# Optimization experiments

Measured on AMD Instinct MI355X. Metric: run time of the kernel, lower is better.

Reference implementation:

```python
import jax, jax.numpy as jnp
import numpy as np

D_MODEL = 1024
N_HEADS = 16
D_K = D_MODEL // N_HEADS
B, S = 4, 2048


def setup_inputs() -> dict:
    key = jax.random.key(0)
    ks = jax.random.split(key, 9)
    sc = 1.0 / np.sqrt(D_MODEL)
    inp = {
        "x": jax.random.normal(ks[0], (B, S, D_MODEL), dtype=jnp.float32),
        # causal mask, broadcastable over batch and heads; 0 -> masked
        "mask": jnp.tril(jnp.ones((S, S), dtype=jnp.int32))[None, None, :, :],
        "Wq": jax.random.normal(ks[1], (D_MODEL, D_MODEL), dtype=jnp.float32) * sc,
        "bq": jax.random.normal(ks[2], (D_MODEL,), dtype=jnp.float32) * sc,
        "Wk": jax.random.normal(ks[3], (D_MODEL, D_MODEL), dtype=jnp.float32) * sc,
        "bk": jax.random.normal(ks[4], (D_MODEL,), dtype=jnp.float32) * sc,
        "Wv": jax.random.normal(ks[5], (D_MODEL, D_MODEL), dtype=jnp.float32) * sc,
        "bv": jax.random.normal(ks[6], (D_MODEL,), dtype=jnp.float32) * sc,
        "Wo": jax.random.normal(ks[7], (D_MODEL, D_MODEL), dtype=jnp.float32) * sc,
        "bo": jax.random.normal(ks[8], (D_MODEL,), dtype=jnp.float32) * sc,
    }
    return inp


def _split_heads(t):
    b, s, _ = t.shape
    return t.reshape(b, s, N_HEADS, D_K).transpose(0, 2, 1, 3)  # [B,H,S,dk]


def reference(x, mask, Wq, bq, Wk, bk, Wv, bv, Wo, bo):
    Q = _split_heads(x @ Wq.T + bq)
    K = _split_heads(x @ Wk.T + bk)
    V = _split_heads(x @ Wv.T + bv)
    scores = jnp.einsum("bhqd,bhkd->bhqk", Q, K) / jnp.sqrt(jnp.float32(D_K))
    scores = jnp.where(mask == 0, jnp.float32(-1e9), scores)
    weights = jax.nn.softmax(scores, axis=-1)
    attn = jnp.einsum("bhqk,bhkd->bhqd", weights, V)  # [B,H,S,dk]
    attn = attn.transpose(0, 2, 1, 3).reshape(x.shape[0], x.shape[1], D_MODEL)
    return attn @ Wo.T + bo
```

## Files before the change

### kernel.cpp

```cpp
#include <hip/hip_runtime.h>
#include <hip/hip_bf16.h>
#include <cstdint>

#define DM   1024
#define NH   16
#define DK   64
#define BB   4
#define SS   2048
#define MTOT (BB * SS)
#define PAD  68

typedef short short8 __attribute__((ext_vector_type(8)));
typedef float f32x4  __attribute__((ext_vector_type(4)));
using u16 = unsigned short;

__device__ inline u16 f2b(float f) {
    union { float f; unsigned int u; } v; v.f = f;
    unsigned int u = v.u;
    u += 0x7fffu + ((u >> 16) & 1u);
    return (u16)(u >> 16);
}
__device__ inline float b2f(u16 s) {
    union { unsigned int u; float f; } v; v.u = ((unsigned int)s) << 16;
    return v.f;
}
__device__ inline unsigned int pack2(float lo, float hi) {
    union { float f; unsigned int u; } a, b; a.f = lo; b.f = hi;
    return (b.u & 0xFFFF0000u) | (a.u >> 16);
}

__device__ inline void load_lds16(const u16* g, u16* l) {
    __builtin_amdgcn_global_load_lds(
        (const __attribute__((address_space(1))) unsigned int*)g,
        (__attribute__((address_space(3))) unsigned int*)l, 16, 0, 0);
}

struct CvtPtrs {
    const void *x, *Wq, *Wk, *Wv, *Wo, *bq, *bk, *bv, *bo;
    u16 *xb, *Wqb, *Wkb, *Wvb, *Wob, *bqb, *bkb, *bvb, *bob;
};

__global__ void convert_all(CvtPtrs p, int* __restrict__ flag)
{
    __shared__ int cnt;
    if (threadIdx.x == 0) cnt = 0;
    __syncthreads();
    int c = 0;
    for (int i = threadIdx.x; i < 512; i += 256) {
        const int e = (((const u16*)p.x)[i] >> 7) & 0xFF;
        if (e >= 100 && e <= 140) c++;
    }
    atomicAdd(&cnt, c);
    __syncthreads();
    const int isbf = (cnt >= 420) ? 1 : 0;
    if (blockIdx.x == 0 && threadIdx.x == 0) *flag = isbf;
    if (isbf) return;

    const size_t E  = (size_t)MTOT * DM;
    const size_t W1 = (size_t)DM * DM;
    const size_t i = ((size_t)blockIdx.x * blockDim.x + threadIdx.x) * 8;
    const float* s; u16* d; size_t off;
    if (i < E) {
        s = (const float*)p.x; d = p.xb; off = i;
    } else {
        size_t j = i - E;
        if (j < (W1 << 2)) {
            const int w = (int)(j >> 20); off = j & (W1 - 1);
            const float* ss[4] = {(const float*)p.Wq, (const float*)p.Wk,
                                  (const float*)p.Wv, (const float*)p.Wo};
            u16* dd[4] = {p.Wqb, p.Wkb, p.Wvb, p.Wob};
            s = ss[w]; d = dd[w];
        } else {
            j -= (W1 << 2);
            if (j >= 4 * DM) return;
            const int w = (int)(j >> 10); off = j & (DM - 1);
            const float* ss[4] = {(const float*)p.bq, (const float*)p.bk,
                                  (const float*)p.bv, (const float*)p.bo};
            u16* dd[4] = {p.bqb, p.bkb, p.bvb, p.bob};
            s = ss[w]; d = dd[w];
        }
    }
    const float4 f0 = *(const float4*)(s + off);
    const float4 f1 = *(const float4*)(s + off + 4);
    u16 tmp[8] = {f2b(f0.x), f2b(f0.y), f2b(f0.z), f2b(f0.w),
                  f2b(f1.x), f2b(f1.y), f2b(f1.z), f2b(f1.w)};
    *(int4*)(d + off) = *(const int4*)tmp;
}

__device__ __forceinline__
void gemm_body(const u16* __restrict__ A, const u16* __restrict__ Bw,
               const u16* __restrict__ bias, void* __restrict__ out,
               int mode, float scale, int isbf, int m0, int n0,
               u16 (*As)[64], u16 (*Bs)[64])
{
    const int tid  = threadIdx.x;
    const int wave = tid >> 6;
    const int lane = tid & 63;
    const int wm = (wave >> 1) * 64;
    const int wn = (wave & 1) * 64;

    const int lm   = lane & 15;
    const int quad = lane >> 4;
    const int kq   = quad * 8;
    const int rq   = quad * 4;

    const int lrow   = lane >> 3;
    const int lchunk = (lane & 7) ^ lrow;
    const u16* gA = A  + (size_t)(m0 + 8*wave + lrow) * DM + lchunk * 8;
    const u16* gB = Bw + (size_t)(n0 + 8*wave + lrow) * DM + lchunk * 8;
    u16* ldsA = (u16*)((char*)&As[0][0] + wave * 1024);
    u16* ldsB = (u16*)((char*)&Bs[0][0] + wave * 1024);

    f32x4 acc[4][4] = {};

    for (int k0 = 0; k0 < DM; k0 += 64) {
        __syncthreads();
#pragma unroll
        for (int c = 0; c < 4; c++) {
            load_lds16(gA + (size_t)c*32*DM + k0, (u16*)((char*)ldsA + c*4096));
            load_lds16(gB + (size_t)c*32*DM + k0, (u16*)((char*)ldsB + c*4096));
        }
        __syncthreads();

#pragma unroll
        for (int ks = 0; ks < 2; ks++) {
            const int ca = ((ks*4 + quad) ^ (lm & 7)) * 8;
            short8 af[4], bf[4];
#pragma unroll
            for (int i = 0; i < 4; i++) af[i] = *(const short8*)(&As[wm + 16*i + lm][ca]);
#pragma unroll
            for (int j = 0; j < 4; j++) bf[j] = *(const short8*)(&Bs[wn + 16*j + lm][ca]);
#pragma unroll
            for (int i = 0; i < 4; i++)
#pragma unroll
                for (int j = 0; j < 4; j++)
                    acc[i][j] = __builtin_amdgcn_mfma_f32_16x16x32_bf16(af[i], bf[j], acc[i][j], 0, 0, 0);
        }
    }

#pragma unroll
    for (int j = 0; j < 4; j++) {
        const int col = n0 + wn + 16*j + lm;
        const float bv = b2f(bias[col]);
        const int h = col >> 6, d = col & 63;
#pragma unroll
        for (int i = 0; i < 4; i++) {
            if (mode == 2) {
                const int row0 = m0 + wm + 16*i + rq;
                const int b = row0 >> 11, s = row0 & 2047;
                u16 tmp[4];
#pragma unroll
                for (int r = 0; r < 4; r++)
                    tmp[r] = f2b((acc[i][j][r] + bv) * scale);
                const size_t idx = (((size_t)(b*NH + h) * DK) + d) * SS + s;
                *(uint2*)(&((u16*)out)[idx]) = *(const uint2*)tmp;
            } else {
#pragma unroll
                for (int r = 0; r < 4; r++) {
                    const int row = m0 + wm + 16*i + rq + r;
                    const float v = (acc[i][j][r] + bv) * scale;
                    if (mode == 0) {
                        const size_t idx = (size_t)row * DM + col;
                        if (isbf) ((u16*)out)[idx] = f2b(v);
                        else      ((float*)out)[idx] = v;
                    } else {
                        const int b = row >> 11, s = row & 2047;
                        const size_t idx = (((size_t)(b*NH + h) * SS) + s) * DK + d;
                        ((u16*)out)[idx] = f2b(v);
                    }
                }
            }
        }
    }
}

__global__ __launch_bounds__(256)
void gemm_qkv(CvtPtrs p, u16* __restrict__ Qb, u16* __restrict__ Kb,
              u16* __restrict__ Vb, float qscale, const int* __restrict__ flag)
{
    __shared__ __align__(16) u16 As[128][64];
    __shared__ __align__(16) u16 Bs[128][64];
    const int id  = blockIdx.x;
    const int xcd = id & 7;
    const int j   = id >> 3;
    const int m0  = (xcd * 8 + (j & 7)) * 128;
    const int n0  = ((j >> 3) & 7) * 128;
    const int z   = j >> 6;
    const int isbf = *flag;
    const u16* A = isbf ? (const u16*)p.x : p.xb;
    const u16* Bw, *bias; u16* out;
    if (z == 0)      { Bw = isbf ? (const u16*)p.Wq : p.Wqb; bias = isbf ? (const u16*)p.bq : p.bqb; out = Qb; }
    else if (z == 1) { Bw = isbf ? (const u16*)p.Wk : p.Wkb; bias = isbf ? (const u16*)p.bk : p.bkb; out = Kb; }
    else             { Bw = isbf ? (const u16*)p.Wv : p.Wvb; bias = isbf ? (const u16*)p.bv : p.bvb; out = Vb; }
    const int mode  = (z == 2) ? 2 : 1;
    const float sc  = (z == 0) ? qscale : 1.0f;
    gemm_body(A, Bw, bias, out, mode, sc, 1, m0, n0, As, Bs);
}

__global__ __launch_bounds__(256)
void gemm_out(const u16* __restrict__ Ab, CvtPtrs p, void* __restrict__ out,
              const int* __restrict__ flag)
{
    __shared__ __align__(16) u16 As[128][64];
    __shared__ __align__(16) u16 Bs[128][64];
    const int id  = blockIdx.x;
    const int xcd = id & 7;
    const int j   = id >> 3;
    const int m0  = (xcd * 8 + (j & 7)) * 128;
    const int n0  = (j >> 3) * 128;
    const int isbf = *flag;
    const u16* Bw   = isbf ? (const u16*)p.Wo : p.Wob;
    const u16* bias = isbf ? (const u16*)p.bo : p.bob;
    gemm_body(Ab, Bw, bias, out, 0, 1.0f, isbf, m0, n0, As, Bs);
}

__global__ __launch_bounds__(256)
void attn_causal(const u16* __restrict__ Q, const u16* __restrict__ K,
                 const u16* __restrict__ VT, u16* __restrict__ O)
{
    __shared__ __align__(16) u16 Ks[2][64][PAD];
    __shared__ __align__(16) u16 Vs[2][64][PAD];
    __shared__ __align__(16) u16 Ps[128][PAD];

    const int tid  = threadIdx.x;
    const int wave = tid >> 6;
    const int lane = tid & 63;
    const int qx = blockIdx.x;
    const int h = blockIdx.y, b = blockIdx.z;
    const int bh = b * NH + h;

    const u16* Kg = K  + (size_t)bh * SS * DK;
    const u16* Vg = VT + (size_t)bh * DK * SS;

    const int srow = tid >> 3;
    const int scol = (tid & 7) * 8;
    const int lm = lane & 15, quad = lane >> 4, kq = quad * 8, rq = quad * 4;

#pragma unroll
    for (int seg = 0; seg < 2; seg++) {
        const int qt = seg ? (15 - qx) : qx;
        const int q0 = qt * 128;
        const int nt = 2 * (qt + 1);
        const u16* Qg = Q + ((size_t)bh * SS + q0) * DK;

        short8 qa[2][2];
#pragma unroll
        for (int mi = 0; mi < 2; mi++)
#pragma unroll
            for (int ks = 0; ks < 2; ks++)
                qa[mi][ks] = *(const short8*)(&Qg[(size_t)(32*wave + 16*mi + lm) * DK + ks*32 + kq]);

        int4 kv0 = *(const int4*)(&Kg[(size_t)srow * DK + scol]);
        int4 kv1 = *(const int4*)(&Kg[(size_t)(srow + 32) * DK + scol]);
        int4 vv0 = *(const int4*)(&Vg[(size_t)srow * SS + scol]);
        int4 vv1 = *(const int4*)(&Vg[(size_t)(srow + 32) * SS + scol]);
        *(int4*)(&Ks[0][srow][scol])      = kv0;
        *(int4*)(&Ks[0][srow + 32][scol]) = kv1;
        *(int4*)(&Vs[0][srow][scol])      = vv0;
        *(int4*)(&Vs[0][srow + 32][scol]) = vv1;
        __syncthreads();

        kv0 = *(const int4*)(&Kg[(size_t)(64 + srow) * DK + scol]);
        kv1 = *(const int4*)(&Kg[(size_t)(64 + srow + 32) * DK + scol]);
        vv0 = *(const int4*)(&Vg[(size_t)srow * SS + 64 + scol]);
        vv1 = *(const int4*)(&Vg[(size_t)(srow + 32) * SS + 64 + scol]);

        f32x4 o[2][4] = {};
        float lacc[2] = {0.f, 0.f};

        for (int t = 0; t < nt; t++) {
            const int buf = t & 1;
            const int k0 = 64 * t;

            f32x4 sw[2][4] = {};
            __builtin_amdgcn_s_setprio(1);
#pragma unroll
            for (int ks = 0; ks < 2; ks++)
#pragma unroll
                for (int j = 0; j < 4; j++) {
                    const short8 kfr = *(const short8*)(&Ks[buf][16*j + lm][ks*32 + kq]);
                    sw[0][j] = __builtin_amdgcn_mfma_f32_16x16x32_bf16(kfr, qa[0][ks], sw[0][j], 0, 0, 0);
                    sw[1][j] = __builtin_amdgcn_mfma_f32_16x16x32_bf16(kfr, qa[1][ks], sw[1][j], 0, 0, 0);
                }
            __builtin_amdgcn_s_setprio(0);

            if (k0 + 63 > q0 + 32*wave) {
#pragma unroll
                for (int mi = 0; mi < 2; mi++)
#pragma unroll
                    for (int j = 0; j < 4; j++)
#pragma unroll
                        for (int r = 0; r < 4; r++)
                            if (k0 + 16*j + rq + r > q0 + 32*wave + 16*mi + lm)
                                sw[mi][j][r] = -1e30f;
            }

#pragma unroll
            for (int mi = 0; mi < 2; mi++) {
#pragma unroll
                for (int j = 0; j < 4; j++) {
                    const float p0 = __builtin_amdgcn_exp2f(sw[mi][j][0]);
                    const float p1 = __builtin_amdgcn_exp2f(sw[mi][j][1]);
                    const float p2 = __builtin_amdgcn_exp2f(sw[mi][j][2]);
                    const float p3 = __builtin_amdgcn_exp2f(sw[mi][j][3]);
                    lacc[mi] += (p0 + p1) + (p2 + p3);
                    uint2 w; w.x = pack2(p0, p1); w.y = pack2(p2, p3);
                    *(uint2*)(&Ps[32*wave + 16*mi + lm][16*j + rq]) = w;
                }
            }

            __builtin_amdgcn_s_setprio(1);
#pragma unroll
            for (int ks = 0; ks < 2; ks++) {
                const short8 pa0 = *(const short8*)(&Ps[32*wave + lm][ks*32 + kq]);
                const short8 pa1 = *(const short8*)(&Ps[32*wave + 16 + lm][ks*32 + kq]);
#pragma unroll
                for (int j = 0; j < 4; j++) {
                    const short8 vfr = *(const short8*)(&Vs[buf][16*j + lm][ks*32 + kq]);
                    o[0][j] = __builtin_amdgcn_mfma_f32_16x16x32_bf16(pa0, vfr, o[0][j], 0, 0, 0);
                    o[1][j] = __builtin_amdgcn_mfma_f32_16x16x32_bf16(pa1, vfr, o[1][j], 0, 0, 0);
                }
            }
            __builtin_amdgcn_s_setprio(0);

            if (t + 1 < nt) {
                const int nb = buf ^ 1;
                *(int4*)(&Ks[nb][srow][scol])      = kv0;
                *(int4*)(&Ks[nb][srow + 32][scol]) = kv1;
                *(int4*)(&Vs[nb][srow][scol])      = vv0;
                *(int4*)(&Vs[nb][srow + 32][scol]) = vv1;
                if (t + 2 < nt) {
                    const int kn = 64 * (t + 2);
                    kv0 = *(const int4*)(&Kg[(size_t)(kn + srow) * DK + scol]);
                    kv1 = *(const int4*)(&Kg[(size_t)(kn + srow + 32) * DK + scol]);
                    vv0 = *(const int4*)(&Vg[(size_t)srow * SS + kn + scol]);
                    vv1 = *(const int4*)(&Vg[(size_t)(srow + 32) * SS + kn + scol]);
                }
            }
            __syncthreads();
        }

#pragma unroll
        for (int mi = 0; mi < 2; mi++) {
            lacc[mi] += __shfl_xor(lacc[mi], 16, 64);
            lacc[mi] += __shfl_xor(lacc[mi], 32, 64);
        }

#pragma unroll
        for (int mi = 0; mi < 2; mi++)
#pragma unroll
            for (int r = 0; r < 4; r++) {
                const float rs = __shfl(lacc[mi], (lane & 48) + rq + r, 64);
                const float inv = 1.f / rs;
                const size_t rowg = (size_t)b * SS + q0 + 32*wave + 16*mi + rq + r;
#pragma unroll
                for (int j = 0; j < 4; j++)
                    O[rowg * DM + h*DK + 16*j + lm] = f2b(o[mi][j][r] * inv);
            }
    }
}

extern "C" void kernel_launch(void* const* d_in, const int* in_sizes, int n_in,
                              void* d_out, int out_size, void* d_ws, size_t ws_size,
                              hipStream_t stream)
{
    (void)in_sizes; (void)n_in; (void)out_size; (void)ws_size;

    int* flag = (int*)d_ws;
    u16* ws = (u16*)((char*)d_ws + 16);

    const size_t E  = (size_t)MTOT * DM;
    const size_t W1 = (size_t)DM * DM;
    u16* xb  = ws;
    u16* Wqb = ws + E;
    u16* Wkb = Wqb + W1;
    u16* Wvb = Wkb + W1;
    u16* Wob = Wvb + W1;
    u16* bqb = Wob + W1;
    u16* bkb = bqb + DM;
    u16* bvb = bkb + DM;
    u16* bob = bvb + DM;
    u16* Qb  = bob + DM;
    u16* Kb  = Qb + E;
    u16* Vb  = Kb + E;
    u16* Ab  = xb;

    CvtPtrs p;
    p.x = d_in[0];
    p.Wq = d_in[2]; p.bq = d_in[3];
    p.Wk = d_in[4]; p.bk = d_in[5];
    p.Wv = d_in[6]; p.bv = d_in[7];
    p.Wo = d_in[8]; p.bo = d_in[9];
    p.xb = xb;
    p.Wqb = Wqb; p.Wkb = Wkb; p.Wvb = Wvb; p.Wob = Wob;
    p.bqb = bqb; p.bkb = bkb; p.bvb = bvb; p.bob = bob;

    const int cvt_blocks = (int)((E + 4*W1 + 4*DM) / 2048);
    convert_all<<<cvt_blocks, 256, 0, stream>>>(p, flag);

    const float qscale = 0.18033688011112042f;

    gemm_qkv<<<1536, 256, 0, stream>>>(p, Qb, Kb, Vb, qscale, flag);
    attn_causal<<<dim3(SS/256, NH, BB), 256, 0, stream>>>(Qb, Kb, Vb, Ab);
    gemm_out<<<512, 256, 0, stream>>>(Ab, p, d_out, flag);
}
```

Before: 285.7 us.

## Load K/V fragments directly from global into registers, drop LDS staging and barriers

The attention kernel no longer stages K and V tiles through shared memory with block-wide barriers. Each wave loads its own MFMA fragments straight from global memory, double-buffering K fragments in registers one tile ahead. Each wave also runs its own causal tile count, so it skips tiles that lie fully above its diagonal. This removes the LDS round trip and the __syncthreads stalls, but each wave now loads K/V redundantly (four times the global/L2 traffic), V loads are not prefetched, and register pressure rises.

```diff
diff --git a/kernel.cpp b/kernel.cpp
--- a/kernel.cpp
+++ b/kernel.cpp
@@ -214,12 +214,79 @@
     gemm_body(Ab, Bw, bias, out, 0, 1.0f, isbf, m0, n0, As, Bs);
 }
 
+
+#define PREF_K(dst, kt) do {                                                    \
+    const int _pk0 = (kt) * 64;                                                 \
+    _Pragma("unroll")                                                           \
+    for (int _pj = 0; _pj < 4; _pj++) {                                         \
+        dst[_pj]     = *(const short8*)(&Kg[(size_t)(_pk0 + 16*_pj + lm)*DK + kq]);      \
+        dst[4 + _pj] = *(const short8*)(&Kg[(size_t)(_pk0 + 16*_pj + lm)*DK + 32 + kq]); \
+    }                                                                           \
+} while (0)
+
+#define TILE_BODY(kt, KF) do {                                                  \
+    const int _k0 = (kt) * 64;                                                  \
+                   \
+    short8 _vf[8];                                                              \
+    _Pragma("unroll")                                                           \
+    for (int _j = 0; _j < 4; _j++) {                                            \
+        _vf[_j]     = *(const short8*)(&Vg[(size_t)(16*_j + lm)*SS + _k0 + kq]);      \
+        _vf[4 + _j] = *(const short8*)(&Vg[(size_t)(16*_j + lm)*SS + _k0 + 32 + kq]); \
+    }                                                                           \
+       \
+    f32x4 _sw[2][4] = {};                                                       \
+    __builtin_amdgcn_s_setprio(1);                                              \
+    _Pragma("unroll")                                                           \
+    for (int _ks = 0; _ks < 2; _ks++)                                           \
+        _Pragma("unroll")                                                       \
+        for (int _j = 0; _j < 4; _j++) {                                        \
+            _sw[0][_j] = __builtin_amdgcn_mfma_f32_16x16x32_bf16(KF[_ks*4+_j], qa[0][_ks], _sw[0][_j], 0, 0, 0); \
+            _sw[1][_j] = __builtin_amdgcn_mfma_f32_16x16x32_bf16(KF[_ks*4+_j], qa[1][_ks], _sw[1][_j], 0, 0, 0); \
+        }                                                                       \
+    __builtin_amdgcn_s_setprio(0);                                              \
+    if (_k0 + 63 > q0 + 32*wave) {                                              \
+        _Pragma("unroll")                                                       \
+        for (int _mi = 0; _mi < 2; _mi++)                                       \
+            _Pragma("unroll")                                                   \
+            for (int _j = 0; _j < 4; _j++)                                      \
+                _Pragma("unroll")                                               \
+                for (int _r = 0; _r < 4; _r++)                                  \
+                    if (_k0 + 16*_j + rq + _r > q0 + 32*wave + 16*_mi + lm)     \
+                        _sw[_mi][_j][_r] = -1e30f;                              \
+    }                                                                           \
+          \
+    _Pragma("unroll")                                                           \
+    for (int _mi = 0; _mi < 2; _mi++) {                                         \
+        _Pragma("unroll")                                                       \
+        for (int _j = 0; _j < 4; _j++) {                                        \
+            const float _p0 = __builtin_amdgcn_exp2f(_sw[_mi][_j][0]);          \
+            const float _p1 = __builtin_amdgcn_exp2f(_sw[_mi][_j][1]);          \
+            const float _p2 = __builtin_amdgcn_exp2f(_sw[_mi][_j][2]);          \
+            const float _p3 = __builtin_amdgcn_exp2f(_sw[_mi][_j][3]);          \
+            lacc[_mi] += (_p0 + _p1) + (_p2 + _p3);                             \
+            uint2 _w; _w.x = pack2(_p0, _p1); _w.y = pack2(_p2, _p3);           \
+            *(uint2*)(&Ps[32*wave + 16*_mi + lm][16*_j + rq]) = _w;             \
+        }                                                                       \
+    }                                                                           \
+                 \
+    __builtin_amdgcn_s_setprio(1);                                              \
+    _Pragma("unroll")                                                           \
+    for (int _ks = 0; _ks < 2; _ks++) {                                         \
+        const short8 _pa0 = *(const short8*)(&Ps[32*wave + lm][_ks*32 + kq]);   \
+        const short8 _pa1 = *(const short8*)(&Ps[32*wave + 16 + lm][_ks*32 + kq]); \
+        _Pragma("unroll")                                                       \
+        for (int _j = 0; _j < 4; _j++) {                                        \
+            o[0][_j] = __builtin_amdgcn_mfma_f32_16x16x32_bf16(_pa0, _vf[_ks*4+_j], o[0][_j], 0, 0, 0); \
+            o[1][_j] = __builtin_amdgcn_mfma_f32_16x16x32_bf16(_pa1, _vf[_ks*4+_j], o[1][_j], 0, 0, 0); \
+        }                                                                       \
+    }                                                                           \
+    __builtin_amdgcn_s_setprio(0);                                              \
+} while (0)
+
 __global__ __launch_bounds__(256)
 void attn_causal(const u16* __restrict__ Q, const u16* __restrict__ K,
                  const u16* __restrict__ VT, u16* __restrict__ O)
 {
-    __shared__ __align__(16) u16 Ks[2][64][PAD];
-    __shared__ __align__(16) u16 Vs[2][64][PAD];
     __shared__ __align__(16) u16 Ps[128][PAD];
 
     const int tid  = threadIdx.x;
@@ -232,15 +299,13 @@
     const u16* Kg = K  + (size_t)bh * SS * DK;
     const u16* Vg = VT + (size_t)bh * DK * SS;
 
-    const int srow = tid >> 3;
-    const int scol = (tid & 7) * 8;
     const int lm = lane & 15, quad = lane >> 4, kq = quad * 8, rq = quad * 4;
 
 #pragma unroll
     for (int seg = 0; seg < 2; seg++) {
         const int qt = seg ? (15 - qx) : qx;
         const int q0 = qt * 128;
-        const int nt = 2 * (qt + 1);
+        const int ntw = (q0 + 32*wave + 95) >> 6;
         const u16* Qg = Q + ((size_t)bh * SS + q0) * DK;
 
         short8 qa[2][2];
@@ -250,94 +315,19 @@
             for (int ks = 0; ks < 2; ks++)
                 qa[mi][ks] = *(const short8*)(&Qg[(size_t)(32*wave + 16*mi + lm) * DK + ks*32 + kq]);
 
-        int4 kv0 = *(const int4*)(&Kg[(size_t)srow * DK + scol]);
-        int4 kv1 = *(const int4*)(&Kg[(size_t)(srow + 32) * DK + scol]);
-        int4 vv0 = *(const int4*)(&Vg[(size_t)srow * SS + scol]);
-        int4 vv1 = *(const int4*)(&Vg[(size_t)(srow + 32) * SS + scol]);
-        *(int4*)(&Ks[0][srow][scol])      = kv0;
-        *(int4*)(&Ks[0][srow + 32][scol]) = kv1;
-        *(int4*)(&Vs[0][srow][scol])      = vv0;
-        *(int4*)(&Vs[0][srow + 32][scol]) = vv1;
-        __syncthreads();
-
-        kv0 = *(const int4*)(&Kg[(size_t)(64 + srow) * DK + scol]);
-        kv1 = *(const int4*)(&Kg[(size_t)(64 + srow + 32) * DK + scol]);
-        vv0 = *(const int4*)(&Vg[(size_t)srow * SS + 64 + scol]);
-        vv1 = *(const int4*)(&Vg[(size_t)(srow + 32) * SS + 64 + scol]);
+        short8 ka[8], kb[8];
+        PREF_K(ka, 0);
 
         f32x4 o[2][4] = {};
         float lacc[2] = {0.f, 0.f};
 
-        for (int t = 0; t < nt; t++) {
-            const int buf = t & 1;
-            const int k0 = 64 * t;
-
-            f32x4 sw[2][4] = {};
-            __builtin_amdgcn_s_setprio(1);
-#pragma unroll
-            for (int ks = 0; ks < 2; ks++)
-#pragma unroll
-                for (int j = 0; j < 4; j++) {
-                    const short8 kfr = *(const short8*)(&Ks[buf][16*j + lm][ks*32 + kq]);
-                    sw[0][j] = __builtin_amdgcn_mfma_f32_16x16x32_bf16(kfr, qa[0][ks], sw[0][j], 0, 0, 0);
-                    sw[1][j] = __builtin_amdgcn_mfma_f32_16x16x32_bf16(kfr, qa[1][ks], sw[1][j], 0, 0, 0);
-                }
-            __builtin_amdgcn_s_setprio(0);
-
-            if (k0 + 63 > q0 + 32*wave) {
-#pragma unroll
-                for (int mi = 0; mi < 2; mi++)
-#pragma unroll
-                    for (int j = 0; j < 4; j++)
-#pragma unroll
-                        for (int r = 0; r < 4; r++)
-                            if (k0 + 16*j + rq + r > q0 + 32*wave + 16*mi + lm)
-                                sw[mi][j][r] = -1e30f;
+        for (int t = 0; t < ntw; t += 2) {
+            if (t + 1 < ntw) PREF_K(kb, t + 1);
+            TILE_BODY(t, ka);
+            if (t + 1 < ntw) {
+                if (t + 2 < ntw) PREF_K(ka, t + 2);
+                TILE_BODY(t + 1, kb);
             }
-
-#pragma unroll
-            for (int mi = 0; mi < 2; mi++) {
-#pragma unroll
-                for (int j = 0; j < 4; j++) {
-                    const float p0 = __builtin_amdgcn_exp2f(sw[mi][j][0]);
-                    const float p1 = __builtin_amdgcn_exp2f(sw[mi][j][1]);
-                    const float p2 = __builtin_amdgcn_exp2f(sw[mi][j][2]);
-                    const float p3 = __builtin_amdgcn_exp2f(sw[mi][j][3]);
-                    lacc[mi] += (p0 + p1) + (p2 + p3);
-                    uint2 w; w.x = pack2(p0, p1); w.y = pack2(p2, p3);
-                    *(uint2*)(&Ps[32*wave + 16*mi + lm][16*j + rq]) = w;
-                }
-            }
-
-            __builtin_amdgcn_s_setprio(1);
-#pragma unroll
-            for (int ks = 0; ks < 2; ks++) {
-                const short8 pa0 = *(const short8*)(&Ps[32*wave + lm][ks*32 + kq]);
-                const short8 pa1 = *(const short8*)(&Ps[32*wave + 16 + lm][ks*32 + kq]);
-#pragma unroll
-                for (int j = 0; j < 4; j++) {
-                    const short8 vfr = *(const short8*)(&Vs[buf][16*j + lm][ks*32 + kq]);
-                    o[0][j] = __builtin_amdgcn_mfma_f32_16x16x32_bf16(pa0, vfr, o[0][j], 0, 0, 0);
-                    o[1][j] = __builtin_amdgcn_mfma_f32_16x16x32_bf16(pa1, vfr, o[1][j], 0, 0, 0);
-                }
-            }
-            __builtin_amdgcn_s_setprio(0);
-
-            if (t + 1 < nt) {
-                const int nb = buf ^ 1;
-                *(int4*)(&Ks[nb][srow][scol])      = kv0;
-                *(int4*)(&Ks[nb][srow + 32][scol]) = kv1;
-                *(int4*)(&Vs[nb][srow][scol])      = vv0;
-                *(int4*)(&Vs[nb][srow + 32][scol]) = vv1;
-                if (t + 2 < nt) {
-                    const int kn = 64 * (t + 2);
-                    kv0 = *(const int4*)(&Kg[(size_t)(kn + srow) * DK + scol]);
-                    kv1 = *(const int4*)(&Kg[(size_t)(kn + srow + 32) * DK + scol]);
-                    vv0 = *(const int4*)(&Vg[(size_t)srow * SS + kn + scol]);
-                    vv1 = *(const int4*)(&Vg[(size_t)(srow + 32) * SS + kn + scol]);
-                }
-            }
-            __syncthreads();
         }
 
 #pragma unroll
```

After: 348.5 us. 1.22x slower.

## Use direct global-to-LDS loads with XOR swizzle and skip fully masked wave tiles

Applied to the files above, without the earlier changes.

Replaces register-staged K/V tile prefetch with direct global-to-LDS async loads (load_lds16) into unpadded, XOR-swizzled shared buffers. The next tile is now issued at the top of each iteration so the copy overlaps compute. Waves whose query rows lie entirely before the key tile now skip the QK, softmax and PV work. This drops register staging and the padding, and cuts causal wasted work per wave. It relies on the load_lds16 helper, defined in lines not shown, and on the swizzle matching the async write pattern.

```diff
diff --git a/kernel.cpp b/kernel.cpp
--- a/kernel.cpp
+++ b/kernel.cpp
@@ -218,8 +218,8 @@
 void attn_causal(const u16* __restrict__ Q, const u16* __restrict__ K,
                  const u16* __restrict__ VT, u16* __restrict__ O)
 {
-    __shared__ __align__(16) u16 Ks[2][64][PAD];
-    __shared__ __align__(16) u16 Vs[2][64][PAD];
+    __shared__ __align__(16) u16 Ks[2][64][64];
+    __shared__ __align__(16) u16 Vs[2][64][64];
     __shared__ __align__(16) u16 Ps[128][PAD];
 
     const int tid  = threadIdx.x;
@@ -232,9 +232,9 @@
     const u16* Kg = K  + (size_t)bh * SS * DK;
     const u16* Vg = VT + (size_t)bh * DK * SS;
 
-    const int srow = tid >> 3;
-    const int scol = (tid & 7) * 8;
     const int lm = lane & 15, quad = lane >> 4, kq = quad * 8, rq = quad * 4;
+    const int lrow   = lane >> 3;
+    const int lchunk = (lane & 7) ^ lrow;
 
 #pragma unroll
     for (int seg = 0; seg < 2; seg++) {
@@ -250,20 +250,13 @@
             for (int ks = 0; ks < 2; ks++)
                 qa[mi][ks] = *(const short8*)(&Qg[(size_t)(32*wave + 16*mi + lm) * DK + ks*32 + kq]);
 
-        int4 kv0 = *(const int4*)(&Kg[(size_t)srow * DK + scol]);
-        int4 kv1 = *(const int4*)(&Kg[(size_t)(srow + 32) * DK + scol]);
-        int4 vv0 = *(const int4*)(&Vg[(size_t)srow * SS + scol]);
-        int4 vv1 = *(const int4*)(&Vg[(size_t)(srow + 32) * SS + scol]);
-        *(int4*)(&Ks[0][srow][scol])      = kv0;
-        *(int4*)(&Ks[0][srow + 32][scol]) = kv1;
-        *(int4*)(&Vs[0][srow][scol])      = vv0;
-        *(int4*)(&Vs[0][srow + 32][scol]) = vv1;
+#pragma unroll
+        for (int c = 0; c < 2; c++) {
+            const int r = 32*c + 8*wave;
+            load_lds16(Kg + (size_t)(r + lrow) * DK + lchunk*8, &Ks[0][r][0]);
+            load_lds16(Vg + (size_t)(r + lrow) * SS + lchunk*8, &Vs[0][r][0]);
+        }
         __syncthreads();
-
-        kv0 = *(const int4*)(&Kg[(size_t)(64 + srow) * DK + scol]);
-        kv1 = *(const int4*)(&Kg[(size_t)(64 + srow + 32) * DK + scol]);
-        vv0 = *(const int4*)(&Vg[(size_t)srow * SS + 64 + scol]);
-        vv1 = *(const int4*)(&Vg[(size_t)(srow + 32) * SS + 64 + scol]);
 
         f32x4 o[2][4] = {};
         float lacc[2] = {0.f, 0.f};
@@ -272,71 +265,70 @@
             const int buf = t & 1;
             const int k0 = 64 * t;
 
-            f32x4 sw[2][4] = {};
-            __builtin_amdgcn_s_setprio(1);
-#pragma unroll
-            for (int ks = 0; ks < 2; ks++)
-#pragma unroll
-                for (int j = 0; j < 4; j++) {
-                    const short8 kfr = *(const short8*)(&Ks[buf][16*j + lm][ks*32 + kq]);
-                    sw[0][j] = __builtin_amdgcn_mfma_f32_16x16x32_bf16(kfr, qa[0][ks], sw[0][j], 0, 0, 0);
-                    sw[1][j] = __builtin_amdgcn_mfma_f32_16x16x32_bf16(kfr, qa[1][ks], sw[1][j], 0, 0, 0);
-                }
-            __builtin_amdgcn_s_setprio(0);
-
-            if (k0 + 63 > q0 + 32*wave) {
-#pragma unroll
-                for (int mi = 0; mi < 2; mi++)
-#pragma unroll
-                    for (int j = 0; j < 4; j++)
-#pragma unroll
-                        for (int r = 0; r < 4; r++)
-                            if (k0 + 16*j + rq + r > q0 + 32*wave + 16*mi + lm)
-                                sw[mi][j][r] = -1e30f;
-            }
-
-#pragma unroll
-            for (int mi = 0; mi < 2; mi++) {
-#pragma unroll
-                for (int j = 0; j < 4; j++) {
-                    const float p0 = __builtin_amdgcn_exp2f(sw[mi][j][0]);
-                    const float p1 = __builtin_amdgcn_exp2f(sw[mi][j][1]);
-                    const float p2 = __builtin_amdgcn_exp2f(sw[mi][j][2]);
-                    const float p3 = __builtin_amdgcn_exp2f(sw[mi][j][3]);
-                    lacc[mi] += (p0 + p1) + (p2 + p3);
-                    uint2 w; w.x = pack2(p0, p1); w.y = pack2(p2, p3);
-                    *(uint2*)(&Ps[32*wave + 16*mi + lm][16*j + rq]) = w;
-                }
-            }
-
-            __builtin_amdgcn_s_setprio(1);
-#pragma unroll
-            for (int ks = 0; ks < 2; ks++) {
-                const short8 pa0 = *(const short8*)(&Ps[32*wave + lm][ks*32 + kq]);
-                const short8 pa1 = *(const short8*)(&Ps[32*wave + 16 + lm][ks*32 + kq]);
-#pragma unroll
-                for (int j = 0; j < 4; j++) {
-                    const short8 vfr = *(const short8*)(&Vs[buf][16*j + lm][ks*32 + kq]);
-                    o[0][j] = __builtin_amdgcn_mfma_f32_16x16x32_bf16(pa0, vfr, o[0][j], 0, 0, 0);
-                    o[1][j] = __builtin_amdgcn_mfma_f32_16x16x32_bf16(pa1, vfr, o[1][j], 0, 0, 0);
-                }
-            }
-            __builtin_amdgcn_s_setprio(0);
-
             if (t + 1 < nt) {
                 const int nb = buf ^ 1;
-                *(int4*)(&Ks[nb][srow][scol])      = kv0;
-                *(int4*)(&Ks[nb][srow + 32][scol]) = kv1;
-                *(int4*)(&Vs[nb][srow][scol])      = vv0;
-                *(int4*)(&Vs[nb][srow + 32][scol]) = vv1;
-                if (t + 2 < nt) {
-                    const int kn = 64 * (t + 2);
-                    kv0 = *(const int4*)(&Kg[(size_t)(kn + srow) * DK + scol]);
-                    kv1 = *(const int4*)(&Kg[(size_t)(kn + srow + 32) * DK + scol]);
-                    vv0 = *(const int4*)(&Vg[(size_t)srow * SS + kn + scol]);
-                    vv1 = *(const int4*)(&Vg[(size_t)(srow + 32) * SS + kn + scol]);
+                const int kn = k0 + 64;
+#pragma unroll
+                for (int c = 0; c < 2; c++) {
+                    const int r = 32*c + 8*wave;
+                    load_lds16(Kg + (size_t)(kn + r + lrow) * DK + lchunk*8, &Ks[nb][r][0]);
+                    load_lds16(Vg + (size_t)(r + lrow) * SS + kn + lchunk*8, &Vs[nb][r][0]);
                 }
             }
+
+            if (k0 <= q0 + 32*wave + 31) {
+                f32x4 sw[2][4] = {};
+                __builtin_amdgcn_s_setprio(1);
+#pragma unroll
+                for (int ks = 0; ks < 2; ks++)
+#pragma unroll
+                    for (int j = 0; j < 4; j++) {
+                        const short8 kfr = *(const short8*)(&Ks[buf][16*j + lm][((ks*4 + quad) ^ (lm & 7)) * 8]);
+                        sw[0][j] = __builtin_amdgcn_mfma_f32_16x16x32_bf16(kfr, qa[0][ks], sw[0][j], 0, 0, 0);
+                        sw[1][j] = __builtin_amdgcn_mfma_f32_16x16x32_bf16(kfr, qa[1][ks], sw[1][j], 0, 0, 0);
+                    }
+                __builtin_amdgcn_s_setprio(0);
+
+                if (k0 + 63 > q0 + 32*wave) {
+#pragma unroll
+                    for (int mi = 0; mi < 2; mi++)
+#pragma unroll
+                        for (int j = 0; j < 4; j++)
+#pragma unroll
+                            for (int r = 0; r < 4; r++)
+                                if (k0 + 16*j + rq + r > q0 + 32*wave + 16*mi + lm)
+                                    sw[mi][j][r] = -1e30f;
+                }
+
+#pragma unroll
+                for (int mi = 0; mi < 2; mi++) {
+#pragma unroll
+                    for (int j = 0; j < 4; j++) {
+                        const float p0 = __builtin_amdgcn_exp2f(sw[mi][j][0]);
+                        const float p1 = __builtin_amdgcn_exp2f(sw[mi][j][1]);
+                        const float p2 = __builtin_amdgcn_exp2f(sw[mi][j][2]);
+                        const float p3 = __builtin_amdgcn_exp2f(sw[mi][j][3]);
+                        lacc[mi] += (p0 + p1) + (p2 + p3);
+                        uint2 w; w.x = pack2(p0, p1); w.y = pack2(p2, p3);
+                        *(uint2*)(&Ps[32*wave + 16*mi + lm][16*j + rq]) = w;
+                    }
+                }
+
+                __builtin_amdgcn_s_setprio(1);
+#pragma unroll
+                for (int ks = 0; ks < 2; ks++) {
+                    const short8 pa0 = *(const short8*)(&Ps[32*wave + lm][ks*32 + kq]);
+                    const short8 pa1 = *(const short8*)(&Ps[32*wave + 16 + lm][ks*32 + kq]);
+#pragma unroll
+                    for (int j = 0; j < 4; j++) {
+                        const short8 vfr = *(const short8*)(&Vs[buf][16*j + lm][((ks*4 + quad) ^ (lm & 7)) * 8]);
+                        o[0][j] = __builtin_amdgcn_mfma_f32_16x16x32_bf16(pa0, vfr, o[0][j], 0, 0, 0);
+                        o[1][j] = __builtin_amdgcn_mfma_f32_16x16x32_bf16(pa1, vfr, o[1][j], 0, 0, 0);
+                    }
+                }
+                __builtin_amdgcn_s_setprio(0);
+            }
+
             __syncthreads();
         }
 
```

Measured after the change: 292.7 us. +2.5%, slower.

## Double-buffer GEMM LDS tiles with K=32 steps to overlap loads and MFMA

Applied to the files above, without the earlier changes.

Reworks the shared GEMM body so that the K loop steps by 32 instead of 64 and keeps two LDS buffers. The next tile is prefetched asynchronously while MFMAs run on the current one, and an XOR swizzle is adapted to the 32-wide rows. Each iteration now needs a single barrier instead of two, but there are twice as many iterations with smaller tiles, so per-iteration overhead increases. The goal is to hide global-to-LDS load latency behind compute in the QKV and output projections.

```diff
diff --git a/kernel.cpp b/kernel.cpp
--- a/kernel.cpp
+++ b/kernel.cpp
@@ -91,7 +91,7 @@
 void gemm_body(const u16* __restrict__ A, const u16* __restrict__ Bw,
                const u16* __restrict__ bias, void* __restrict__ out,
                int mode, float scale, int isbf, int m0, int n0,
-               u16 (*As)[64], u16 (*Bs)[64])
+               u16 (*As)[128][32], u16 (*Bs)[128][32])
 {
     const int tid  = threadIdx.x;
     const int wave = tid >> 6;
@@ -101,41 +101,50 @@
 
     const int lm   = lane & 15;
     const int quad = lane >> 4;
-    const int kq   = quad * 8;
     const int rq   = quad * 4;
 
-    const int lrow   = lane >> 3;
-    const int lchunk = (lane & 7) ^ lrow;
-    const u16* gA = A  + (size_t)(m0 + 8*wave + lrow) * DM + lchunk * 8;
-    const u16* gB = Bw + (size_t)(n0 + 8*wave + lrow) * DM + lchunk * 8;
-    u16* ldsA = (u16*)((char*)&As[0][0] + wave * 1024);
-    u16* ldsB = (u16*)((char*)&Bs[0][0] + wave * 1024);
+    const int caf = ((quad ^ (lm & 3) ^ ((lm >> 2) & 3)) * 8);
+
+    const int lrow0 = 32*wave + (lane >> 2);
+    const int chs   = (((lane & 3) ^ ((lane >> 2) & 3) ^ ((lane >> 4) & 3)) * 8);
+    const u16* gA0 = A  + (size_t)(m0 + lrow0)      * DM + chs;
+    const u16* gA1 = A  + (size_t)(m0 + lrow0 + 16) * DM + chs;
+    const u16* gB0 = Bw + (size_t)(n0 + lrow0)      * DM + chs;
+    const u16* gB1 = Bw + (size_t)(n0 + lrow0 + 16) * DM + chs;
 
     f32x4 acc[4][4] = {};
 
-    for (int k0 = 0; k0 < DM; k0 += 64) {
-        __syncthreads();
-#pragma unroll
-        for (int c = 0; c < 4; c++) {
-            load_lds16(gA + (size_t)c*32*DM + k0, (u16*)((char*)ldsA + c*4096));
-            load_lds16(gB + (size_t)c*32*DM + k0, (u16*)((char*)ldsB + c*4096));
+    load_lds16(gA0, &As[0][32*wave][0]);
+    load_lds16(gA1, &As[0][32*wave + 16][0]);
+    load_lds16(gB0, &Bs[0][32*wave][0]);
+    load_lds16(gB1, &Bs[0][32*wave + 16][0]);
+    __syncthreads();
+
+#pragma unroll 2
+    for (int h = 0; h < 32; ++h) {
+        const int cb = h & 1;
+
+        if (h + 1 < 32) {
+            const int nb = cb ^ 1;
+            const int kn = (h + 1) * 32;
+            load_lds16(gA0 + kn, &As[nb][32*wave][0]);
+            load_lds16(gA1 + kn, &As[nb][32*wave + 16][0]);
+            load_lds16(gB0 + kn, &Bs[nb][32*wave][0]);
+            load_lds16(gB1 + kn, &Bs[nb][32*wave + 16][0]);
         }
-        __syncthreads();
-
-#pragma unroll
-        for (int ks = 0; ks < 2; ks++) {
-            const int ca = ((ks*4 + quad) ^ (lm & 7)) * 8;
-            short8 af[4], bf[4];
-#pragma unroll
-            for (int i = 0; i < 4; i++) af[i] = *(const short8*)(&As[wm + 16*i + lm][ca]);
-#pragma unroll
-            for (int j = 0; j < 4; j++) bf[j] = *(const short8*)(&Bs[wn + 16*j + lm][ca]);
-#pragma unroll
-            for (int i = 0; i < 4; i++)
-#pragma unroll
-                for (int j = 0; j < 4; j++)
-                    acc[i][j] = __builtin_amdgcn_mfma_f32_16x16x32_bf16(af[i], bf[j], acc[i][j], 0, 0, 0);
-        }
+
+        short8 af[4], bf[4];
+#pragma unroll
+        for (int i = 0; i < 4; i++) af[i] = *(const short8*)(&As[cb][wm + 16*i + lm][caf]);
+#pragma unroll
+        for (int j = 0; j < 4; j++) bf[j] = *(const short8*)(&Bs[cb][wn + 16*j + lm][caf]);
+#pragma unroll
+        for (int i = 0; i < 4; i++)
+#pragma unroll
+            for (int j = 0; j < 4; j++)
+                acc[i][j] = __builtin_amdgcn_mfma_f32_16x16x32_bf16(af[i], bf[j], acc[i][j], 0, 0, 0);
+
+        if (h + 1 < 32) __syncthreads();
     }
 
 #pragma unroll
@@ -178,8 +187,8 @@
 void gemm_qkv(CvtPtrs p, u16* __restrict__ Qb, u16* __restrict__ Kb,
               u16* __restrict__ Vb, float qscale, const int* __restrict__ flag)
 {
-    __shared__ __align__(16) u16 As[128][64];
-    __shared__ __align__(16) u16 Bs[128][64];
+    __shared__ __align__(16) u16 As[2][128][32];
+    __shared__ __align__(16) u16 Bs[2][128][32];
     const int id  = blockIdx.x;
     const int xcd = id & 7;
     const int j   = id >> 3;
@@ -201,8 +210,8 @@
 void gemm_out(const u16* __restrict__ Ab, CvtPtrs p, void* __restrict__ out,
               const int* __restrict__ flag)
 {
-    __shared__ __align__(16) u16 As[128][64];
-    __shared__ __align__(16) u16 Bs[128][64];
+    __shared__ __align__(16) u16 As[2][128][32];
+    __shared__ __align__(16) u16 Bs[2][128][32];
     const int id  = blockIdx.x;
     const int xcd = id & 7;
     const int j   = id >> 3;
```

Result: slower. 321.1 us (+12.4%).
